# Kernel optimization log

Measured on AMD Instinct MI355X. Metric: run time of the kernel, lower is better.

Reference implementation:

```python
import jax, jax.numpy as jnp
import numpy as np

B, H, W = 16, 16, 16
DIM = 768
NH = 8
HD = DIM // NH
NEXP = 8
TOPK = 2
DSTATE = 1
DTRANK = 4
KDIR = 4


def setup_inputs() -> dict:
    key = jax.random.key(0)
    ks = jax.random.split(key, 16)
    s = 1.0 / float(np.sqrt(DIM))
    inp = {
        'x': jax.random.normal(ks[0], (B, H, W, DIM)),
        'sa_in_w': jax.random.normal(ks[1], (3 * DIM, DIM)) * s,
        'sa_in_b': jnp.zeros((3 * DIM,)),
        'sa_out_w': jax.random.normal(ks[2], (DIM, DIM)) * s,
        'sa_out_b': jnp.zeros((DIM,)),
        'ca_in_w': jax.random.normal(ks[3], (2 * DIM, DIM)) * s,
        'ca_in_b': jnp.zeros((2 * DIM,)),
        'expert_queries': jax.random.normal(ks[4], (NEXP, DIM)) * s,
        'e_in_w': jax.random.normal(ks[5], (NEXP, 2 * DIM, DIM)) * s,
        'e_in_b': jnp.zeros((NEXP, 2 * DIM)),
        'e_conv_w': jax.random.normal(ks[6], (NEXP, DIM, 1, 3, 3)) / 3.0,
        'e_conv_b': jnp.zeros((NEXP, DIM)),
        'e_xproj_w': jax.random.normal(ks[7], (NEXP, KDIR, DTRANK + 2 * DSTATE, DIM)) * s,
        'e_dtproj_w': jax.random.normal(ks[8], (NEXP, KDIR, DIM, DTRANK)) * 0.1,
        'e_dtproj_b': jax.random.uniform(ks[9], (NEXP, KDIR, DIM), minval=-4.0, maxval=-2.0),
        'e_Alog': jax.random.uniform(ks[10], (NEXP, KDIR, DIM, DSTATE), minval=0.0, maxval=1.0),
        'e_D': jnp.ones((NEXP, KDIR, DIM)),
        'e_ln_scale': jnp.ones((NEXP, DIM)),
        'e_ln_bias': jnp.zeros((NEXP, DIM)),
    }
    return {k: v.astype(jnp.float32) for k, v in inp.items()}


def _selective_scan(xs, Wx, Wdt, bdt, Alog, D):
    # xs: [B, L, d]; Wx: [R+2N, d]; Wdt: [d, R]; Alog: [d, N]; D: [d]
    dbl = jnp.einsum('bld,ed->ble', xs, Wx)
    dt = jax.nn.softplus(jnp.einsum('blr,dr->bld', dbl[..., :DTRANK], Wdt) + bdt)
    Bm = dbl[..., DTRANK:DTRANK + DSTATE]
    Cm = dbl[..., DTRANK + DSTATE:]
    A = -jnp.exp(Alog)  # [d, N]

    def step(h, t):
        dt_t, B_t, C_t, x_t = t  # [b,d],[b,N],[b,N],[b,d]
        h = jnp.exp(dt_t[:, :, None] * A) * h + (dt_t * x_t)[:, :, None] * B_t[:, None, :]
        return h, jnp.einsum('bdn,bn->bd', h, C_t)

    b, L, d = xs.shape
    h0 = jnp.zeros((b, d, DSTATE), xs.dtype)
    tm = lambda a: jnp.moveaxis(a, 1, 0)
    _, ys = jax.lax.scan(step, h0, (tm(dt), tm(Bm), tm(Cm), tm(xs)))
    return jnp.moveaxis(ys, 0, 1) + D * xs


def _expert(in_w, in_b, conv_w, conv_b, xproj_w, dtp_w, dtp_b, Alog, D, ln_s, ln_b, x):
    b = x.shape[0]
    xz = jnp.einsum('bhwc,oc->bhwo', x, in_w) + in_b
    xc, z = jnp.split(xz, 2, axis=-1)
    xn = jax.lax.conv_general_dilated(jnp.transpose(xc, (0, 3, 1, 2)), conv_w,
                                      (1, 1), ((1, 1), (1, 1)), feature_group_count=DIM)
    xc = jax.nn.silu(jnp.transpose(xn + conv_b[None, :, None, None], (0, 2, 3, 1)))
    L = H * W
    xh = xc.reshape(b, L, DIM)                              # row-major 'h'
    xv = jnp.transpose(xc, (0, 2, 1, 3)).reshape(b, L, DIM)  # col-major 'v'
    seqs = jnp.stack([xh, xh[:, ::-1], xv, xv[:, ::-1]])     # [4, b, L, d]
    ys = jax.vmap(_selective_scan)(seqs, xproj_w, dtp_w, dtp_b, Alog, D)
    yv = ys[2] + ys[3][:, ::-1]
    yv = jnp.transpose(yv.reshape(b, W, H, DIM), (0, 2, 1, 3)).reshape(b, L, DIM)
    y = (ys[0] + ys[1][:, ::-1] + yv).reshape(b, H, W, DIM)
    mu = y.mean(-1, keepdims=True)
    var = ((y - mu) ** 2).mean(-1, keepdims=True)
    y = (y - mu) * jax.lax.rsqrt(var + 1e-5) * ln_s + ln_b   # out_norm (LayerNorm)
    y = y * jax.nn.silu(z)
    return y.mean((1, 2))  # AdaptiveAvgPool2d((1,1)) -> [b, DIM]


def _forward(x, sa_in_w, sa_in_b, sa_out_w, sa_out_b, ca_in_w, ca_in_b, expert_queries,
             e_in_w, e_in_b, e_conv_w, e_conv_b, e_xproj_w, e_dtproj_w, e_dtproj_b,
             e_Alog, e_D, e_ln_scale, e_ln_bias):
    b = x.shape[0]
    L = H * W
    scale = 1.0 / float(np.sqrt(HD))
    xs = x.reshape(b, L, DIM)
    # spatial self-attention (eval mode: dropout off)
    qkv = xs @ sa_in_w.T + sa_in_b
    q, k, v = [a.reshape(b, L, NH, HD) for a in jnp.split(qkv, 3, -1)]
    att = jax.nn.softmax(jnp.einsum('bqhd,bkhd->bhqk', q, k) * scale, -1)
    ctx = jnp.einsum('bhqk,bkhd->bqhd', att, v).reshape(b, L, DIM) @ sa_out_w.T + sa_out_b
    # expert cross-attention: only head-averaged attention weights are used
    q2 = (ctx @ ca_in_w[:DIM].T + ca_in_b[:DIM]).reshape(b, L, NH, HD)
    k2 = (expert_queries @ ca_in_w[DIM:].T + ca_in_b[DIM:]).reshape(NEXP, NH, HD)
    aw = jax.nn.softmax(jnp.einsum('blhd,ehd->bhle', q2, k2) * scale, -1).mean(1)  # [b,L,E]
    gate = jax.nn.softmax(aw.mean(1), -1)  # [b, E]
    tk_scores, tk_idx = jax.lax.top_k(gate, TOPK)
    wgt = jax.nn.softmax(tk_scores, -1)
    # dense expert compute (all experts on all samples), then gather top-k
    all_out = jax.vmap(_expert, in_axes=(0,) * 11 + (None,))(
        e_in_w, e_in_b, e_conv_w, e_conv_b, e_xproj_w, e_dtproj_w, e_dtproj_b,
        e_Alog, e_D, e_ln_scale, e_ln_bias, x)  # [E, b, DIM]
    per_b = jnp.transpose(all_out, (1, 0, 2))  # [b, E, DIM]
    sel = jnp.take_along_axis(per_b, tk_idx[:, :, None], axis=1)  # [b, K, DIM]
    return jnp.sum(wgt[:, :, None] * sel, axis=1)  # [b, DIM]


def reference(x, sa_in_w, sa_in_b, sa_out_w, sa_out_b, ca_in_w, ca_in_b, expert_queries,
              e_in_w, e_in_b, e_conv_w, e_conv_b, e_xproj_w, e_dtproj_w, e_dtproj_b,
              e_Alog, e_D, e_ln_scale, e_ln_bias):
    return _forward(x, sa_in_w, sa_in_b, sa_out_w, sa_out_b, ca_in_w, ca_in_b, expert_queries,
                    e_in_w, e_in_b, e_conv_w, e_conv_b, e_xproj_w, e_dtproj_w, e_dtproj_b,
                    e_Alog, e_D, e_ln_scale, e_ln_bias)
```

## Files before the change

### kernel.cpp

```cpp
#include <hip/hip_runtime.h>
#include <hip/hip_bf16.h>


#define LTOK 256
#define DIMC 768

typedef unsigned short ushortt;
typedef __attribute__((ext_vector_type(8))) short bf16x8;
typedef __attribute__((ext_vector_type(4))) float f32x4;

#define LOG2E 1.44269504f
#define LN2   0.69314718f

__device__ __forceinline__ float fexp2(float x) { return __builtin_amdgcn_exp2f(x); }
__device__ __forceinline__ float flog2(float x) { return __builtin_amdgcn_logf(x); }

__device__ __forceinline__ ushortt f2b(float f) {
  union { float f; unsigned u; } c; c.f = f;
  unsigned r = (c.u + 0x7FFFu + ((c.u >> 16) & 1u)) >> 16;
  return (ushortt)r;
}

__global__ __launch_bounds__(256) void mk_mcast4(
    const float* __restrict__ s0, ushortt* __restrict__ d0,
    const float* __restrict__ s1, ushortt* __restrict__ d1,
    const float* __restrict__ s2, ushortt* __restrict__ d2,
    const float* __restrict__ s3, ushortt* __restrict__ d3)
{
  long g = (long)blockIdx.x * 256 + threadIdx.x;
  const float* s; ushortt* dst; long o;
  if (g < 786432)       { s = s0; dst = d0; o = g; }
  else if (g < 1228800) { s = s1; dst = d1; o = g - 786432; }
  else if (g < 1376256) { s = s2; dst = d2; o = g - 1228800; }
  else                  { s = s3; dst = d3; o = g - 1376256; }
  o <<= 2;
  float4 v = *(const float4*)(s + o);
  ushort4 w;
  w.x = f2b(v.x); w.y = f2b(v.y); w.z = f2b(v.z); w.w = f2b(v.w);
  *(ushort4*)(dst + o) = w;
}

__global__ __launch_bounds__(256) void mk_cast(const float* __restrict__ in,
                                               ushortt* __restrict__ outp, long n)
{
  long i = ((long)blockIdx.x * 256 + threadIdx.x) * 4;
  if (i + 3 < n) {
    float4 v = *(const float4*)(in + i);
    ushort4 o;
    o.x = f2b(v.x); o.y = f2b(v.y); o.z = f2b(v.z); o.w = f2b(v.w);
    *(ushort4*)(outp + i) = o;
  }
}

__global__ __launch_bounds__(256) void mk_mfma(
    const ushortt* __restrict__ A, const ushortt* __restrict__ B,
    const float* __restrict__ bias, void* __restrict__ C,
    int K, int lda, int ldb, int ldc,
    int zdiv, long sA1, long sA2, long sB1, long sB2, long sC1, long sC2,
    long sBias,
    const int* __restrict__ pairExp, int tilesN,
    int outBf, int splitN, void* __restrict__ C2, int ldc2, int outBf2, int c2vt)
{
  int z = blockIdx.y;
  long aoff, boff, coff, biasoff = 0;
  if (pairExp) {
    int e = pairExp[z];
    aoff = (long)(z >> 1) * sA1; boff = (long)e * sB1;
    coff = (long)z * sC1; biasoff = (long)e * sBias;
  } else {
    int z1 = z / zdiv, z2 = z - z1 * zdiv;
    aoff = (long)z1 * sA1 + (long)z2 * sA2;
    boff = (long)z1 * sB1 + (long)z2 * sB2;
    coff = (long)z1 * sC1 + (long)z2 * sC2;
  }
  int tile = blockIdx.x;
  int tm = tile / tilesN, tn = tile - tm * tilesN;
  long m0 = (long)tm << 7, n0 = (long)tn << 7;

  __shared__ ushortt As[128][40];
  __shared__ ushortt Bs[128][40];

  int tid = threadIdx.x;
  int lane = tid & 63, wvi = tid >> 6;
  int wr = wvi >> 1, wc = wvi & 1;
  int lm = lane & 15, lg = lane >> 4;

  f32x4 zero4 = {0.f, 0.f, 0.f, 0.f};
  f32x4 acc[4][4];
#pragma unroll
  for (int i = 0; i < 4; i++)
#pragma unroll
    for (int j = 0; j < 4; j++) acc[i][j] = zero4;

  const ushortt* Ab = A + aoff;
  const ushortt* Bb = B + boff;

  for (int k0 = 0; k0 < K; k0 += 32) {
#pragma unroll
    for (int h = 0; h < 2; h++) {
      int q = tid + h * 256;
      int row = q >> 2, ck = (q & 3) << 3;
      *(uint4*)&As[row][ck] = *(const uint4*)(Ab + (m0 + row) * lda + k0 + ck);
      *(uint4*)&Bs[row][ck] = *(const uint4*)(Bb + (n0 + row) * ldb + k0 + ck);
    }
    __syncthreads();
    bf16x8 af[4], bfr[4];
#pragma unroll
    for (int i = 0; i < 4; i++)
      af[i] = *(const bf16x8*)&As[wr * 64 + i * 16 + lm][lg << 3];
#pragma unroll
    for (int j = 0; j < 4; j++)
      bfr[j] = *(const bf16x8*)&Bs[wc * 64 + j * 16 + lm][lg << 3];
#pragma unroll
    for (int i = 0; i < 4; i++)
#pragma unroll
      for (int j = 0; j < 4; j++)
        acc[i][j] = __builtin_amdgcn_mfma_f32_16x16x32_bf16(af[i], bfr[j], acc[i][j], 0, 0, 0);
    __syncthreads();
  }

#pragma unroll
  for (int mt = 0; mt < 4; mt++) {
#pragma unroll
    for (int nt = 0; nt < 4; nt++) {
      long grow = m0 + wr * 64 + mt * 16 + lg * 4;
      long gcol = n0 + wc * 64 + nt * 16 + lm;
      float bv = bias ? bias[biasoff + gcol] : 0.f;
      if ((int)gcol < splitN) {
#pragma unroll
        for (int r = 0; r < 4; r++) {
          float v = acc[mt][nt][r] + bv;
          long idx = coff + (grow + r) * ldc + gcol;
          if (outBf) ((ushortt*)C)[idx] = f2b(v);
          else ((float*)C)[idx] = v;
        }
      } else if (c2vt) {
        int cc = (int)gcol - splitN;
        int hh = cc / 96, jj = cc - hh * 96;
#pragma unroll
        for (int r = 0; r < 4; r++) {
          float v = acc[mt][nt][r] + bv;
          long gr = grow + r;
          long b = gr >> 8, t = gr & 255;
          long idx = (((b * 8 + hh) * 128 + jj) << 8) + t;
          ((ushortt*)C2)[idx] = f2b(v);
        }
      } else {
        long col = gcol - splitN;
#pragma unroll
        for (int r = 0; r < 4; r++) {
          float v = acc[mt][nt][r] + bv;
          long idx = coff + (grow + r) * ldc2 + col;
          if (outBf2) ((ushortt*)C2)[idx] = f2b(v);
          else ((float*)C2)[idx] = v;
        }
      }
    }
  }
}

__global__ __launch_bounds__(256) void mk_gemm(
    const float* __restrict__ A, const float* __restrict__ B,
    const float* __restrict__ bias, float* __restrict__ C,
    int M, int N, int K, int lda, int ldb, int ldc, int tilesN)
{
  int tile = blockIdx.x;
  int tm = tile / tilesN, tn = tile - tm * tilesN;
  int m0 = tm << 6, n0 = tn << 6;

  __shared__ float As[16][68];
  __shared__ float Bs[16][68];

  int tid = threadIdx.x;
  int tx = tid & 15, ty = tid >> 4;
  int lrow = tid >> 2;
  int lk = (tid & 3) << 2;

  float acc[4][4];
#pragma unroll
  for (int i = 0; i < 4; i++)
#pragma unroll
    for (int j = 0; j < 4; j++) acc[i][j] = 0.f;

  for (int k0 = 0; k0 < K; k0 += 16) {
    {
      int gm = m0 + lrow;
      float4 v = {0.f, 0.f, 0.f, 0.f};
      if (gm < M) v = *(const float4*)(A + (long)gm * lda + (k0 + lk));
      As[lk + 0][lrow] = v.x; As[lk + 1][lrow] = v.y;
      As[lk + 2][lrow] = v.z; As[lk + 3][lrow] = v.w;
    }
    {
      int gn = n0 + lrow;
      float4 v = {0.f, 0.f, 0.f, 0.f};
      if (gn < N) v = *(const float4*)(B + (long)gn * ldb + (k0 + lk));
      Bs[lk + 0][lrow] = v.x; Bs[lk + 1][lrow] = v.y;
      Bs[lk + 2][lrow] = v.z; Bs[lk + 3][lrow] = v.w;
    }
    __syncthreads();
#pragma unroll
    for (int kk = 0; kk < 16; kk++) {
      float4 a = *(const float4*)&As[kk][ty << 2];
      float4 b = *(const float4*)&Bs[kk][tx << 2];
      acc[0][0] += a.x * b.x; acc[0][1] += a.x * b.y; acc[0][2] += a.x * b.z; acc[0][3] += a.x * b.w;
      acc[1][0] += a.y * b.x; acc[1][1] += a.y * b.y; acc[1][2] += a.y * b.z; acc[1][3] += a.y * b.w;
      acc[2][0] += a.z * b.x; acc[2][1] += a.z * b.y; acc[2][2] += a.z * b.z; acc[2][3] += a.z * b.w;
      acc[3][0] += a.w * b.x; acc[3][1] += a.w * b.y; acc[3][2] += a.w * b.z; acc[3][3] += a.w * b.w;
    }
    __syncthreads();
  }

#pragma unroll
  for (int i = 0; i < 4; i++) {
    int gm = m0 + (ty << 2) + i;
    if (gm >= M) continue;
#pragma unroll
    for (int j = 0; j < 4; j++) {
      int gn = n0 + (tx << 2) + j;
      if (gn >= N) continue;
      float v = acc[i][j];
      if (bias) v += bias[gn];
      C[(long)gm * ldc + gn] = v;
    }
  }
}

__global__ __launch_bounds__(256) void mk_softmax(const float* __restrict__ scores,
                                                  ushortt* __restrict__ att, float scale)
{
  int row = (blockIdx.x << 2) + (threadIdx.x >> 6);
  int lane = threadIdx.x & 63;
  const float* p = scores + (long)row * 256 + (lane << 2);
  float4 v = *(const float4*)p;
  float m = fmaxf(fmaxf(v.x, v.y), fmaxf(v.z, v.w));
#pragma unroll
  for (int o = 32; o; o >>= 1) m = fmaxf(m, __shfl_xor(m, o, 64));
  float sl = scale * LOG2E;
  v.x = fexp2(sl * (v.x - m));
  v.y = fexp2(sl * (v.y - m));
  v.z = fexp2(sl * (v.z - m));
  v.w = fexp2(sl * (v.w - m));
  float s = v.x + v.y + v.z + v.w;
#pragma unroll
  for (int o = 32; o; o >>= 1) s += __shfl_xor(s, o, 64);
  float r = 1.f / s;
  ushort4 o4;
  o4.x = f2b(v.x * r); o4.y = f2b(v.y * r); o4.z = f2b(v.z * r); o4.w = f2b(v.w * r);
  *(ushort4*)(att + (long)row * 256 + (lane << 2)) = o4;
}

__global__ __launch_bounds__(256) void mk_gates(const float* __restrict__ q2,
                                                const float* __restrict__ k2,
                                                float* __restrict__ gacc)
{
  __shared__ float k2p[8 * 808];
  int b = blockIdx.x >> 4, q = blockIdx.x & 15;
  for (int i = threadIdx.x; i < 6144; i += 256) {
    int e = i / 768, rem = i - e * 768;
    int h = rem / 96, j = rem - h * 96;
    k2p[e * 808 + h * 100 + j] = k2[i];
  }
  __syncthreads();
  const float scale = 0.10206207261596577f;
  int wid = threadIdx.x >> 6, lane = threadIdx.x & 63;
  int h = lane >> 3, e = lane & 7;
  const float* kp = &k2p[e * 808 + h * 100];
  float accL = 0.f;
#pragma unroll
  for (int ti = 0; ti < 4; ti++) {
    int l = q * 16 + wid * 4 + ti;
    const float* qh = q2 + ((long)b * LTOK + l) * DIMC + h * 96;
    float sum = 0.f;
#pragma unroll
    for (int j = 0; j < 96; j += 4) {
      float4 qv = *(const float4*)(qh + j);
      float4 kv = *(const float4*)(kp + j);
      sum += qv.x * kv.x + qv.y * kv.y + qv.z * kv.z + qv.w * kv.w;
    }
    float s = sum * scale;
    float mx = s;
#pragma unroll
    for (int o = 1; o <= 4; o <<= 1) mx = fmaxf(mx, __shfl_xor(mx, o, 64));
    float ex = fexp2((s - mx) * LOG2E);
    float se = ex;
#pragma unroll
    for (int o = 1; o <= 4; o <<= 1) se += __shfl_xor(se, o, 64);
    accL += ex / se;
  }
#pragma unroll
  for (int o = 8; o <= 32; o <<= 1) accL += __shfl_xor(accL, o, 64);
  __shared__ float red[4][8];
  if (lane < 8) red[wid][lane] = accL;
  __syncthreads();
  if (threadIdx.x < 8) {
    float v = red[0][threadIdx.x] + red[1][threadIdx.x] +
              red[2][threadIdx.x] + red[3][threadIdx.x];
    atomicAdd(&gacc[b * 8 + threadIdx.x], v);
  }
}

__global__ __launch_bounds__(64) void mk_gatetop(const float* __restrict__ gacc,
                                                 int* __restrict__ pe,
                                                 float* __restrict__ pw)
{
  int b = threadIdx.x;
  if (b >= 16) return;
  float g[8];
  for (int e = 0; e < 8; e++) g[e] = gacc[b * 8 + e] * (1.f / (8.f * 256.f));
  float mx = g[0];
  for (int e = 1; e < 8; e++) mx = fmaxf(mx, g[e]);
  float se = 0.f;
  for (int e = 0; e < 8; e++) { g[e] = expf(g[e] - mx); se += g[e]; }
  for (int e = 0; e < 8; e++) g[e] /= se;
  int i0 = 0;
  for (int e = 1; e < 8; e++) if (g[e] > g[i0]) i0 = e;
  int i1 = (i0 == 0) ? 1 : 0;
  for (int e = 0; e < 8; e++) if (e != i0 && g[e] > g[i1]) i1 = e;
  float w0 = 1.f / (1.f + expf(g[i1] - g[i0]));
  pe[2 * b] = i0; pe[2 * b + 1] = i1;
  pw[2 * b] = w0; pw[2 * b + 1] = 1.f - w0;
}

__global__ __launch_bounds__(768) void mk_conv(const float* __restrict__ xzx,
                                               const float* __restrict__ cw,
                                               const float* __restrict__ cb,
                                               const int* __restrict__ pe,
                                               float* __restrict__ xc)
{
  int blk = blockIdx.x;
  int p = blk >> 8, t = blk & 255;
  int e = pe[p];
  int h = t >> 4, w = t & 15;
  int c = threadIdx.x;
  const float* wp = cw + ((long)e * DIMC + c) * 9;
  float acc = cb[e * DIMC + c];
#pragma unroll
  for (int dh = 0; dh < 3; dh++) {
    int hh = h + dh - 1;
    if (hh < 0 || hh > 15) continue;
#pragma unroll
    for (int dw = 0; dw < 3; dw++) {
      int ww = w + dw - 1;
      if (ww < 0 || ww > 15) continue;
      acc += xzx[((long)p * LTOK + hh * 16 + ww) * DIMC + c] * wp[dh * 3 + dw];
    }
  }
  xc[((long)p * LTOK + t) * DIMC + c] = acc / (1.f + fexp2(-acc * LOG2E));
}

__device__ __forceinline__ int tmap(int dir, int s) {
  if (dir == 0) return s;
  if (dir == 1) return 255 - s;
  if (dir == 2) return ((s & 15) << 4) | (s >> 4);
  int u = 255 - s;
  return ((u & 15) << 4) | (u >> 4);
}

__global__ __launch_bounds__(256) void mk_dbl(const float* __restrict__ xc,
                                              const float* __restrict__ xproj,
                                              const int* __restrict__ pe,
                                              float* __restrict__ dblm)
{
  int p = blockIdx.x >> 6;
  int tq = blockIdx.x & 63;
  int wid = threadIdx.x >> 6, lane = threadIdx.x & 63;
  int m = tq * 4 + wid;
  int e = pe[p];
  const float* xr = xc + ((long)p * LTOK + m) * DIMC;
  const float* wb = xproj + (long)e * 24 * DIMC;
  float4 xv[3];
#pragma unroll
  for (int j = 0; j < 3; j++) xv[j] = *(const float4*)(xr + j * 256 + lane * 4);
  float acc[24];
#pragma unroll
  for (int r = 0; r < 24; r++) {
    const float* wr = wb + r * DIMC;
    float s = 0.f;
#pragma unroll
    for (int j = 0; j < 3; j++) {
      float4 wv = *(const float4*)(wr + j * 256 + lane * 4);
      s += xv[j].x * wv.x + xv[j].y * wv.y + xv[j].z * wv.z + xv[j].w * wv.w;
    }
    acc[r] = s;
  }
#pragma unroll
  for (int r = 0; r < 24; r++)
#pragma unroll
    for (int o = 32; o; o >>= 1) acc[r] += __shfl_xor(acc[r], o, 64);
  if (lane == 0) {
    float* o = dblm + ((long)p * LTOK + m) * 32;
#pragma unroll
    for (int r = 0; r < 24; r++) o[(r / 6) * 8 + (r - (r / 6) * 6)] = acc[r];
  }
}

__global__ __launch_bounds__(512, 4) void mk_scan(const float* __restrict__ xc,
                                               const float* __restrict__ dblm,
                                               const float* __restrict__ dtw,
                                               const float* __restrict__ dtb,
                                               const float* __restrict__ Alog,
                                               const float* __restrict__ Dp,
                                               const int* __restrict__ pe,
                                               float* __restrict__ yac)
{
  __shared__ __attribute__((aligned(16))) float dbS[256 * 36];
  __shared__ float yS[256 * 17];
  __shared__ __attribute__((aligned(16))) float xS[256 * 20];
  __shared__ float ahS[32][16][2];
  __shared__ float dsum[16];
  int blk = blockIdx.x;
  int p = blk / 48, cg = blk - p * 48;
  int c0 = cg << 4;
  int e = pe[p];
  int tid = threadIdx.x;
  {
    const float4* src = (const float4*)(dblm + (long)p * LTOK * 32);
    for (int i = tid; i < 2048; i += 512) {
      int t = i >> 3, c4 = i & 7;
      int rot = (t >> 5) & 7;
      *(float4*)&dbS[t * 36 + (((c4 + rot) & 7) << 2)] = src[i];
    }
  }
  {
    const float* xcp = xc + (long)p * LTOK * DIMC + c0;
    for (int i = tid; i < 1024; i += 512) {
      int t = i >> 2, c4 = i & 3;
      *(float4*)&xS[t * 20 + (((t >> 5) & 1) << 2) + (c4 << 2)] =
          *(const float4*)(xcp + (long)t * DIMC + (c4 << 2));
    }
  }
  for (int i = tid; i < 256 * 17; i += 512) yS[i] = 0.f;
  if (tid < 16) {
    float s = 0.f;
#pragma unroll
    for (int dd = 0; dd < 4; dd++) s += Dp[(long)(e * 4 + dd) * DIMC + c0 + tid];
    dsum[tid] = s;
  }
  __syncthreads();

  int c = tid & 15;
  int rr = tid >> 4;
  int seg = rr & 7;
  int dir = rr >> 3;
  int d = c0 + c;
  long pb = (long)(e * 4 + dir) * DIMC + d;
  float4 wv = *(const float4*)(dtw + pb * 4);
  float bdt = dtb[pb];
  float Ad = -fexp2(Alog[pb] * LOG2E);
  int t0 = seg << 5;
  int stp = (dir == 0) ? 1 : (dir == 1) ? -1 : (dir == 2) ? 16 : -16;

  float de[32], inc[32];
  float h = 0.f, ap = 1.f;
#pragma unroll
  for (int tb = 0; tb < 32; tb += 8) {
    int mb = tmap(dir, t0 + tb);
#pragma unroll
    for (int i = 0; i < 8; i++) {
      int mm = mb + i * stp;
      int rot = (mm >> 5) & 7;
      float4 dv = *(const float4*)&dbS[mm * 36 + (((dir * 2 + rot) & 7) << 2)];
      float Bv = dbS[mm * 36 + (((dir * 2 + 1 + rot) & 7) << 2)];
      float xl = (wv.x * dv.x + wv.y * dv.y + wv.z * dv.z + wv.w * dv.w + bdt) * LOG2E;
      float te = fexp2(xl);
      float g = flog2(1.f + te);
      g = (xl > 86.f) ? xl : g;
      float dei = fexp2(g * Ad);
      float xsv = xS[mm * 20 + (((mm >> 5) & 1) << 2) + c];
      float inci = (g * LN2) * xsv * Bv;
      de[tb + i] = dei; inc[tb + i] = inci;
      h = dei * h + inci;
      ap *= dei;
    }
  }
  ahS[rr][c][0] = ap;
  ahS[rr][c][1] = h;
  __syncthreads();

  float hh = 0.f;
  {
    int base = dir << 3;
    float av[8], hv[8];
#pragma unroll
    for (int j = 0; j < 8; j++) {
      av[j] = ahS[base + j][c][0];
      hv[j] = ahS[base + j][c][1];
    }
#pragma unroll
    for (int j = 0; j < 7; j++)
      if (j < seg) hh = av[j] * hh + hv[j];
  }

#pragma unroll
  for (int tb = 0; tb < 32; tb += 8) {
    int mb = tmap(dir, t0 + tb);
#pragma unroll
    for (int i = 0; i < 8; i++) {
      int mm = mb + i * stp;
      int rot = (mm >> 5) & 7;
      float cv = dbS[mm * 36 + (((dir * 2 + 1 + rot) & 7) << 2) + 1];
      hh = de[tb + i] * hh + inc[tb + i];
      atomicAdd(&yS[mm * 17 + c], hh * cv);
    }
  }
  __syncthreads();

  float* yp = yac + (long)p * LTOK * DIMC + c0;
  for (int i = tid; i < 4096; i += 512) {
    int t = i >> 4, cz = i & 15;
    yp[(long)t * DIMC + cz] = yS[t * 17 + cz] +
        xS[t * 20 + (((t >> 5) & 1) << 2) + cz] * dsum[cz];
  }
}

__global__ __launch_bounds__(256) void mk_lnfin(const float* __restrict__ yac,
                                                const float* __restrict__ xzz,
                                                const float* __restrict__ lns,
                                                const float* __restrict__ lnb,
                                                const int* __restrict__ pe,
                                                float* __restrict__ eo)
{
  int blk = blockIdx.x;
  int p = blk >> 4, ts = blk & 15;
  int e = pe[p];
  int tid = threadIdx.x;
  int wid = tid >> 6, lane = tid & 63;
  float ls[12], lb[12], acc[12];
#pragma unroll
  for (int i = 0; i < 12; i++) {
    int d = i * 64 + lane;
    ls[i] = lns[e * DIMC + d];
    lb[i] = lnb[e * DIMC + d];
    acc[i] = 0.f;
  }
#pragma unroll
  for (int tt = 0; tt < 4; tt++) {
    int t = ts * 16 + wid * 4 + tt;
    const float* yr = yac + ((long)p * LTOK + t) * DIMC;
    const float* zr = xzz + ((long)p * LTOK + t) * DIMC;
    float v[12];
    float s = 0.f;
#pragma unroll
    for (int i = 0; i < 12; i++) { v[i] = yr[i * 64 + lane]; s += v[i]; }
#pragma unroll
    for (int o = 32; o; o >>= 1) s += __shfl_xor(s, o, 64);
    float mu = s * (1.f / 768.f);
    float sq = 0.f;
#pragma unroll
    for (int i = 0; i < 12; i++) { float dlt = v[i] - mu; sq += dlt * dlt; }
#pragma unroll
    for (int o = 32; o; o >>= 1) sq += __shfl_xor(sq, o, 64);
    float rs = rsqrtf(sq * (1.f / 768.f) + 1e-5f);
#pragma unroll
    for (int i = 0; i < 12; i++) {
      float y = (v[i] - mu) * rs * ls[i] + lb[i];
      float z = zr[i * 64 + lane];
      y *= z / (1.f + fexp2(-z * LOG2E));
      acc[i] += y;
    }
  }
  __shared__ float sacc[768];
  for (int j = tid; j < 768; j += 256) sacc[j] = 0.f;
  __syncthreads();
#pragma unroll
  for (int i = 0; i < 12; i++) atomicAdd(&sacc[i * 64 + lane], acc[i]);
  __syncthreads();
  for (int j = tid; j < 768; j += 256) atomicAdd(&eo[(long)p * DIMC + j], sacc[j]);
}

__global__ __launch_bounds__(768) void mk_out(const float* __restrict__ eo,
                                              const float* __restrict__ pw,
                                              float* __restrict__ out)
{
  int b = blockIdx.x, d = threadIdx.x;
  float v = pw[2 * b] * eo[(long)(2 * b) * DIMC + d] +
            pw[2 * b + 1] * eo[(long)(2 * b + 1) * DIMC + d];
  out[b * DIMC + d] = v * (1.f / 256.f);
}

extern "C" void kernel_launch(void* const* d_in, const int* in_sizes, int n_in,
                              void* d_out, int out_size, void* d_ws, size_t ws_size,
                              hipStream_t stream)
{
  const float* x        = (const float*)d_in[0];
  const float* sa_in_w  = (const float*)d_in[1];
  const float* sa_in_b  = (const float*)d_in[2];
  const float* sa_out_w = (const float*)d_in[3];
  const float* sa_out_b = (const float*)d_in[4];
  const float* ca_in_w  = (const float*)d_in[5];
  const float* ca_in_b  = (const float*)d_in[6];
  const float* eq       = (const float*)d_in[7];
  const float* e_in_w   = (const float*)d_in[8];
  const float* e_in_b   = (const float*)d_in[9];
  const float* e_conv_w = (const float*)d_in[10];
  const float* e_conv_b = (const float*)d_in[11];
  const float* e_xproj  = (const float*)d_in[12];
  const float* e_dtw    = (const float*)d_in[13];
  const float* e_dtb    = (const float*)d_in[14];
  const float* e_Alog   = (const float*)d_in[15];
  const float* e_D      = (const float*)d_in[16];
  const float* e_lns    = (const float*)d_in[17];
  const float* e_lnb    = (const float*)d_in[18];
  float* out = (float*)d_out;

  float* ws = (float*)d_ws;
  ushortt* qk_b   = (ushortt*)(ws + 0);
  float*   scores = ws + 6291456;
  ushortt* dump_b = (ushortt*)(ws + 6291456);
  ushortt* ctxa_b = (ushortt*)(ws + 7864320);
  ushortt* att_b  = (ushortt*)(ws + 14680064);
  ushortt* vt_b   = (ushortt*)(ws + 18874368);
  ushortt* xb     = (ushortt*)(ws + 20971520);
  ushortt* wqkv_b = (ushortt*)(ws + 22544384);
  ushortt* saow_b = (ushortt*)(ws + 23429120);
  ushortt* caw_b  = (ushortt*)(ws + 23724032);
  ushortt* ctx_b  = (ushortt*)(ws + 0);
  float*   q2     = ws + 1572864;
  float*   k2     = ws + 25165824;
  int*     pe     = (int*)(ws + 25171968);
  float*   pw     = ws + 25172000;
  float*   eo     = ws + 25172032;
  float*   gacc   = ws + 25393216;
  float*   xz_x   = ws + 0;
  float*   xz_z   = ws + 6291456;
  ushortt* ew_b   = (ushortt*)(ws + 12582912);
  float*   xc     = ws + 12582912;
  float*   yac    = ws + 18874368;
  float*   dblm   = ws + 0;

  const float scale = 0.10206207261596577f;

  mk_mcast4<<<5952, 256, 0, stream>>>(x, xb, sa_in_w, wqkv_b, sa_out_w, saow_b,
                                      ca_in_w, caw_b);
  mk_mfma<<<dim3(576, 1), 256, 0, stream>>>(xb, wqkv_b, sa_in_b, qk_b,
      768, 768, 768, 1536, 1, 0, 0, 0, 0, 0, 0, 0, nullptr, 18,
      1, 1536, vt_b, 0, 1, 1);
  mk_mfma<<<dim3(4, 128), 256, 0, stream>>>(qk_b, qk_b + 768, nullptr, scores,
      96, 1536, 1536, 256, 8, 393216, 96, 393216, 96, 524288, 65536, 0, nullptr, 2,
      0, 1 << 30, nullptr, 0, 0, 0);
  mk_softmax<<<8192, 256, 0, stream>>>(scores, att_b, scale);
  mk_mfma<<<dim3(2, 128), 256, 0, stream>>>(att_b, vt_b, nullptr, ctxa_b,
      256, 256, 256, 768, 8, 524288, 65536, 262144, 32768, 196608, 96, 0, nullptr, 1,
      1, 96, dump_b, 32, 1, 0);
  mk_cast<<<9216, 256, 0, stream>>>(e_in_w, ew_b, 9437184);
  mk_mfma<<<dim3(192, 1), 256, 0, stream>>>(ctxa_b, saow_b, sa_out_b, ctx_b,
      768, 768, 768, 768, 1, 0, 0, 0, 0, 0, 0, 0, nullptr, 6,
      1, 1 << 30, nullptr, 0, 0, 0);
  mk_mfma<<<dim3(192, 1), 256, 0, stream>>>(ctx_b, caw_b, ca_in_b, q2,
      768, 768, 768, 768, 1, 0, 0, 0, 0, 0, 0, 0, nullptr, 6,
      0, 1 << 30, nullptr, 0, 0, 0);
  mk_gemm<<<dim3(12, 1), 256, 0, stream>>>(eq, ca_in_w + 589824, ca_in_b + 768, k2,
      8, 768, 768, 768, 768, 768, 12);
  (void)hipMemsetAsync(gacc, 0, 128 * sizeof(float), stream);
  (void)hipMemsetAsync(eo, 0, 24576 * sizeof(float), stream);
  mk_gates<<<256, 256, 0, stream>>>(q2, k2, gacc);
  mk_gatetop<<<1, 64, 0, stream>>>(gacc, pe, pw);
  mk_mfma<<<dim3(24, 32), 256, 0, stream>>>(xb, ew_b, e_in_b, xz_x,
      768, 768, 768, 768, 1, 196608, 0, 1179648, 0, 196608, 0, 1536, pe, 12,
      0, 768, xz_z, 768, 0, 0);
  mk_conv<<<32 * 256, 768, 0, stream>>>(xz_x, e_conv_w, e_conv_b, pe, xc);
  mk_dbl<<<2048, 256, 0, stream>>>(xc, e_xproj, pe, dblm);
  mk_scan<<<1536, 512, 0, stream>>>(xc, dblm, e_dtw, e_dtb, e_Alog, e_D, pe, yac);
  mk_lnfin<<<512, 256, 0, stream>>>(yac, xz_z, e_lns, e_lnb, pe, eo);
  mk_out<<<16, 768, 0, stream>>>(eo, pw, out);

  (void)in_sizes; (void)n_in; (void)out_size; (void)ws_size;
}
```

Before: 667.3 us.

## Split chunked scan output into local and carry-in terms to avoid recurrence replay

The chunked selective scan now writes the local-chunk output contribution during the first pass. It stores only the cumulative decay times C per step and adds carry-in times that product in the second pass, instead of keeping two per-step arrays and replaying the recurrence. This lowers register pressure and serial work in the second pass, and B and C are now read as one float2. The cost is twice as many LDS atomic adds per element, and the padding swizzle moves from xS to yS.

```diff
diff --git a/kernel.cpp b/kernel.cpp
--- a/kernel.cpp
+++ b/kernel.cpp
@@ -404,8 +404,8 @@
                                                float* __restrict__ yac)
 {
   __shared__ __attribute__((aligned(16))) float dbS[256 * 36];
-  __shared__ float yS[256 * 17];
-  __shared__ __attribute__((aligned(16))) float xS[256 * 20];
+  __shared__ __attribute__((aligned(16))) float xS[256 * 16];
+  __shared__ __attribute__((aligned(16))) float yS[256 * 20];
   __shared__ float ahS[32][16][2];
   __shared__ float dsum[16];
   int blk = blockIdx.x;
@@ -425,11 +425,14 @@
     const float* xcp = xc + (long)p * LTOK * DIMC + c0;
     for (int i = tid; i < 1024; i += 512) {
       int t = i >> 2, c4 = i & 3;
-      *(float4*)&xS[t * 20 + (((t >> 5) & 1) << 2) + (c4 << 2)] =
+      *(float4*)&xS[t * 16 + (c4 << 2)] =
           *(const float4*)(xcp + (long)t * DIMC + (c4 << 2));
     }
   }
-  for (int i = tid; i < 256 * 17; i += 512) yS[i] = 0.f;
+  {
+    float4 z4 = {0.f, 0.f, 0.f, 0.f};
+    for (int i = tid; i < 1280; i += 512) ((float4*)yS)[i] = z4;
+  }
   if (tid < 16) {
     float s = 0.f;
 #pragma unroll
@@ -450,7 +453,7 @@
   int t0 = seg << 5;
   int stp = (dir == 0) ? 1 : (dir == 1) ? -1 : (dir == 2) ? 16 : -16;
 
-  float de[32], inc[32];
+  float pc[32];
   float h = 0.f, ap = 1.f;
 #pragma unroll
   for (int tb = 0; tb < 32; tb += 8) {
@@ -460,17 +463,17 @@
       int mm = mb + i * stp;
       int rot = (mm >> 5) & 7;
       float4 dv = *(const float4*)&dbS[mm * 36 + (((dir * 2 + rot) & 7) << 2)];
-      float Bv = dbS[mm * 36 + (((dir * 2 + 1 + rot) & 7) << 2)];
+      float2 bc = *(const float2*)&dbS[mm * 36 + (((dir * 2 + 1 + rot) & 7) << 2)];
       float xl = (wv.x * dv.x + wv.y * dv.y + wv.z * dv.z + wv.w * dv.w + bdt) * LOG2E;
       float te = fexp2(xl);
       float g = flog2(1.f + te);
       g = (xl > 86.f) ? xl : g;
-      float dei = fexp2(g * Ad);
-      float xsv = xS[mm * 20 + (((mm >> 5) & 1) << 2) + c];
-      float inci = (g * LN2) * xsv * Bv;
-      de[tb + i] = dei; inc[tb + i] = inci;
-      h = dei * h + inci;
-      ap *= dei;
+      float de = fexp2(g * Ad);
+      float xsv = xS[mm * 16 + c];
+      h = de * h + (g * LN2) * xsv * bc.x;
+      ap *= de;
+      pc[tb + i] = ap * bc.y;
+      atomicAdd(&yS[mm * 20 + c + (((mm >> 5) & 1) << 2)], h * bc.y);
     }
   }
   ahS[rr][c][0] = ap;
@@ -497,10 +500,7 @@
 #pragma unroll
     for (int i = 0; i < 8; i++) {
       int mm = mb + i * stp;
-      int rot = (mm >> 5) & 7;
-      float cv = dbS[mm * 36 + (((dir * 2 + 1 + rot) & 7) << 2) + 1];
-      hh = de[tb + i] * hh + inc[tb + i];
-      atomicAdd(&yS[mm * 17 + c], hh * cv);
+      atomicAdd(&yS[mm * 20 + c + (((mm >> 5) & 1) << 2)], pc[tb + i] * hh);
     }
   }
   __syncthreads();
@@ -508,8 +508,8 @@
   float* yp = yac + (long)p * LTOK * DIMC + c0;
   for (int i = tid; i < 4096; i += 512) {
     int t = i >> 4, cz = i & 15;
-    yp[(long)t * DIMC + cz] = yS[t * 17 + cz] +
-        xS[t * 20 + (((t >> 5) & 1) << 2) + cz] * dsum[cz];
+    yp[(long)t * DIMC + cz] = yS[t * 20 + cz + (((t >> 5) & 1) << 2)] +
+        xS[t * 16 + cz] * dsum[cz];
   }
 }
 
```

Measured after the change: 747.1 us. +11.9%, slower.
